# Kernel tuning notes

Measured on AMD Instinct MI355X. Metric: run time of the kernel, lower is better.

## Reference

```python
import jax, jax.numpy as jnp
import numpy as np

N_USERS = 50000
N_ENTITIES = 100000
N_EDGES = 2000000
NNZ = 1000000
N_REL = 17  # n_relations; weight has n_relations-1 = 16 rows
DIM = 64
N_HOPS = 3


def setup_inputs() -> dict:
    key = jax.random.key(0)
    ks = jax.random.split(key, 8)
    user_emb = jax.random.normal(ks[0], (N_USERS, DIM), dtype=jnp.float32)
    entity_emb = jax.random.normal(ks[1], (N_ENTITIES, DIM), dtype=jnp.float32)
    weight = jax.random.normal(ks[2], (N_REL - 1, DIM), dtype=jnp.float32)
    unmask = jax.random.uniform(ks[3], (N_EDGES,), dtype=jnp.float32)
    edge_index = jax.random.randint(ks[4], (2, N_EDGES), 0, N_ENTITIES, dtype=jnp.int64) if jax.config.jax_enable_x64 else jax.random.randint(ks[4], (2, N_EDGES), 0, N_ENTITIES).astype(jnp.int32)
    edge_type = jax.random.randint(ks[5], (N_EDGES,), 1, N_REL).astype(edge_index.dtype)
    interact_rows = jax.random.randint(ks[6], (NNZ,), 0, N_USERS).astype(edge_index.dtype)
    interact_cols = jax.random.randint(ks[7], (NNZ,), 0, N_ENTITIES).astype(edge_index.dtype)
    return {
        "user_emb": user_emb,
        "entity_emb": entity_emb,
        "weight": weight,
        "unmask": unmask,
        "edge_index": edge_index,
        "edge_type": edge_type,
        "interact_rows": interact_rows,
        "interact_cols": interact_cols,
    }


def _l2_normalize(x, eps=1e-12):
    # matches torch.nn.functional.normalize(dim=1)
    norm = jnp.sqrt(jnp.sum(x * x, axis=1, keepdims=True))
    return x / jnp.maximum(norm, eps)


def reference(user_emb, entity_emb, weight, unmask, edge_index, edge_type, interact_rows, interact_cols):
    """GraphConv.forward with mess_dropout=False, node_dropout=False (eval math)."""
    head = edge_index[0]
    tail = edge_index[1]
    rel_emb = weight[edge_type - 1]                      # [E, D] gather
    entity_res = entity_emb
    user_res = user_emb
    ent = entity_emb
    for _ in range(N_HOPS):
        # KG aggregate: gather-multiply-scatter_sum
        neigh = ent[tail] * unmask[:, None] * rel_emb    # [E, D]
        ent_agg = jax.ops.segment_sum(neigh, head, num_segments=N_ENTITIES)
        # user aggregate: sparse (unit-valued COO) mm -> gather + segment_sum
        usr_agg = jax.ops.segment_sum(ent[interact_cols], interact_rows, num_segments=N_USERS)
        ent = _l2_normalize(ent_agg)
        usr = _l2_normalize(usr_agg)
        entity_res = entity_res + ent
        user_res = user_res + usr
    return entity_res, user_res
```

## Files before the change

### kernel.cpp

```cpp
#include <hip/hip_runtime.h>
#include <hip/hip_fp16.h>
#include <math.h>

#define N_USERS   50000
#define N_ENT     100000
#define N_EDGES   2000000
#define NNZ       1000000
#define DIM       64
#define HALF_E    (N_ENT / 2)
#define HALF_U    (N_USERS / 2)

#define GA      512
#define NB_E    391
#define NB_U    196
#define NALL_E  (NB_E * GA)
#define NALL_U  (NB_U * GA)
#define NALL    (NALL_E + NALL_U)
#define NB_SCAN (NALL / 512)
#define CAP_D   6400


__device__ inline unsigned pack_h2(float x, float y) {
    unsigned lo = __half_as_ushort(__float2half_rn(x));
    unsigned hi = __half_as_ushort(__float2half_rn(y));
    return lo | (hi << 16);
}

__device__ inline float2 unpack_h2(unsigned u) {
    __half2 h = *reinterpret_cast<__half2*>(&u);
    return __half22float2(h);
}

__device__ inline __half2 bits_h2(unsigned u) { return *reinterpret_cast<__half2*>(&u); }

__device__ inline __half2 shfl_h2(__half2 v, int o) {
    int x = *reinterpret_cast<int*>(&v);
    x = __shfl_xor(x, o, 64);
    return *reinterpret_cast<__half2*>(&x);
}

__global__ void f32_to_f16(const float4* __restrict__ in, uint4* __restrict__ out, int n4) {
    int i = blockIdx.x * blockDim.x + threadIdx.x;
    if (i < n4) {
        float4 a = in[2 * i], b = in[2 * i + 1];
        uint4 o;
        o.x = pack_h2(a.x, a.y);
        o.y = pack_h2(a.z, a.w);
        o.z = pack_h2(b.x, b.y);
        o.w = pack_h2(b.z, b.w);
        out[i] = o;
    }
}


__global__ __launch_bounds__(256) void bucket_hist_both(
    const int* __restrict__ head, const int* __restrict__ irows, int* __restrict__ bh) {
    __shared__ int h[NB_E];
    bool isE = blockIdx.x < GA;
    int b = isE ? blockIdx.x : blockIdx.x - GA;
    const int* key = isE ? head : irows;
    int n = isE ? N_EDGES : NNZ;
    int nbuck = isE ? NB_E : NB_U;
    int base = isE ? 0 : NALL_E;
    for (int t = threadIdx.x; t < nbuck; t += 256) h[t] = 0;
    __syncthreads();
    int chunk = (n + GA - 1) / GA;
    int s = b * chunk;
    int e = n < s + chunk ? n : s + chunk;
    for (int i = s + threadIdx.x; i < e; i += 256)
        atomicAdd(&h[key[i] >> 8], 1);
    __syncthreads();
    for (int t = threadIdx.x; t < nbuck; t += 256)
        bh[base + t * GA + b] = h[t];
}

__global__ void scan_partial(const int* __restrict__ cnt, int n, int* __restrict__ bsum) {
    __shared__ int sd[512];
    int tid = threadIdx.x, i = blockIdx.x * 512 + tid;
    sd[tid] = (i < n) ? cnt[i] : 0;
    __syncthreads();
    for (int s = 256; s > 0; s >>= 1) {
        if (tid < s) sd[tid] += sd[tid + s];
        __syncthreads();
    }
    if (tid == 0) bsum[blockIdx.x] = sd[0];
}

__global__ void scan_bsum(int* bsum, int nb) {
    __shared__ int sd[1024];
    int tid = threadIdx.x;
    int v = (tid < nb) ? bsum[tid] : 0;
    sd[tid] = v;
    __syncthreads();
    for (int o = 1; o < 1024; o <<= 1) {
        int t = (tid >= o) ? sd[tid - o] : 0;
        __syncthreads();
        sd[tid] += t;
        __syncthreads();
    }
    if (tid < nb) bsum[tid] = sd[tid] - v;
}

__global__ void scan_final(const int* __restrict__ cnt, int n,
                           const int* __restrict__ bsum, int* __restrict__ rp) {
    __shared__ int sd[512];
    int tid = threadIdx.x, i = blockIdx.x * 512 + tid;
    int v = (i < n) ? cnt[i] : 0;
    sd[tid] = v;
    __syncthreads();
    for (int o = 1; o < 512; o <<= 1) {
        int t = (tid >= o) ? sd[tid - o] : 0;
        __syncthreads();
        sd[tid] += t;
        __syncthreads();
    }
    int incl = sd[tid] + bsum[blockIdx.x];
    if (i < n) rp[i] = incl - v;
    if (i == n - 1) rp[n] = incl;
}

__global__ __launch_bounds__(256) void bucket_scatter_both(
    const int* __restrict__ head, const int* __restrict__ tail,
    const int* __restrict__ etype, const float* __restrict__ unmask,
    const int* __restrict__ irows, const int* __restrict__ icols,
    const int* __restrict__ off, long long* __restrict__ tmp_ev,
    int* __restrict__ tmp_col) {
    __shared__ int h[NB_E];
    __shared__ int boff[NB_E];
    bool isE = blockIdx.x < GA;
    int b = isE ? blockIdx.x : blockIdx.x - GA;
    if (isE) {
        for (int t = threadIdx.x; t < NB_E; t += 256) { h[t] = 0; boff[t] = off[t * GA + b]; }
        __syncthreads();
        int chunk = (N_EDGES + GA - 1) / GA;
        int s = b * chunk;
        int e = N_EDGES < s + chunk ? N_EDGES : s + chunk;
        for (int i = s + threadIdx.x; i < e; i += 256) {
            int k = head[i];
            int bk = k >> 8;
            int local = atomicAdd(&h[bk], 1);
            unsigned hh = __half_as_ushort(__float2half_rn(unmask[i]));
            unsigned hi = hh | (hh << 16);
            unsigned lo = (unsigned)(tail[i] | ((etype[i] - 1) << 20) | ((k & 255) << 24));
            tmp_ev[boff[bk] + local] = (long long)(((unsigned long long)hi << 32) | lo);
        }
    } else {
        for (int t = threadIdx.x; t < NB_U; t += 256) { h[t] = 0; boff[t] = off[NALL_E + t * GA + b] - N_EDGES; }
        __syncthreads();
        int chunk = (NNZ + GA - 1) / GA;
        int s = b * chunk;
        int e = NNZ < s + chunk ? NNZ : s + chunk;
        for (int i = s + threadIdx.x; i < e; i += 256) {
            int k = irows[i];
            int bk = k >> 8;
            int local = atomicAdd(&h[bk], 1);
            tmp_col[boff[bk] + local] = icols[i] | ((k & 255) << 24);
        }
    }
}

__global__ __launch_bounds__(256) void bucket_sort_both(
    const int* __restrict__ off, const long long* __restrict__ tmp_ev,
    const int* __restrict__ tmp_col, long long* __restrict__ ev,
    int* __restrict__ col_s, int* __restrict__ rp_e, int* __restrict__ rp_u) {
    __shared__ int khist[256];
    __shared__ int koff[256];
    __shared__ long long stage[CAP_D];
    int t = threadIdx.x;
    bool isE = blockIdx.x < NB_E;
    if (isE) {
        int b = blockIdx.x;
        int sb = off[b * GA], se = off[(b + 1) * GA];
        int len = se - sb;
        khist[t] = 0;
        __syncthreads();
        for (int i = t; i < len; i += 256)
            atomicAdd(&khist[(int)(((unsigned long long)tmp_ev[sb + i] >> 24) & 255)], 1);
        __syncthreads();
        int v = khist[t];
        koff[t] = v;
        __syncthreads();
        for (int o = 1; o < 256; o <<= 1) {
            int x = (t >= o) ? koff[t - o] : 0;
            __syncthreads();
            koff[t] += x;
            __syncthreads();
        }
        int excl = koff[t] - v;
        int key = b * 256 + t;
        if (key < N_ENT) rp_e[key] = sb + excl;
        if (b == 0 && t == 0) rp_e[N_ENT] = N_EDGES;
        khist[t] = excl;
        __syncthreads();
        if (len <= CAP_D) {
            for (int i = t; i < len; i += 256) {
                long long v2 = tmp_ev[sb + i];
                int k = (int)(((unsigned long long)v2 >> 24) & 255);
                int p = atomicAdd(&khist[k], 1);
                stage[p] = v2;
            }
            __syncthreads();
            for (int i = t; i < len; i += 256)
                ev[sb + i] = stage[i] & (long long)0xFFFFFFFF00FFFFFFULL;
        } else {
            for (int i = t; i < len; i += 256) {
                long long v2 = tmp_ev[sb + i];
                int k = (int)(((unsigned long long)v2 >> 24) & 255);
                int p = atomicAdd(&khist[k], 1);
                ev[sb + p] = v2 & (long long)0xFFFFFFFF00FFFFFFULL;
            }
        }
    } else {
        int b = blockIdx.x - NB_E;
        int sb = off[NALL_E + b * GA] - N_EDGES;
        int se = off[NALL_E + (b + 1) * GA] - N_EDGES;
        int len = se - sb;
        int* stage32 = (int*)stage;
        khist[t] = 0;
        __syncthreads();
        for (int i = t; i < len; i += 256)
            atomicAdd(&khist[(tmp_col[sb + i] >> 24) & 255], 1);
        __syncthreads();
        int v = khist[t];
        koff[t] = v;
        __syncthreads();
        for (int o = 1; o < 256; o <<= 1) {
            int x = (t >= o) ? koff[t - o] : 0;
            __syncthreads();
            koff[t] += x;
            __syncthreads();
        }
        int excl = koff[t] - v;
        int key = b * 256 + t;
        if (key < N_USERS) rp_u[key] = sb + excl;
        if (b == 0 && t == 0) rp_u[N_USERS] = NNZ;
        khist[t] = excl;
        __syncthreads();
        if (len <= CAP_D) {
            for (int i = t; i < len; i += 256) {
                int v2 = tmp_col[sb + i];
                int p = atomicAdd(&khist[(v2 >> 24) & 255], 1);
                stage32[p] = v2;
            }
            __syncthreads();
            for (int i = t; i < len; i += 256)
                col_s[sb + i] = stage32[i] & 0x00FFFFFF;
        } else {
            for (int i = t; i < len; i += 256) {
                int v2 = tmp_col[sb + i];
                int p = atomicAdd(&khist[(v2 >> 24) & 255], 1);
                col_s[sb + p] = v2 & 0x00FFFFFF;
            }
        }
    }
}


__device__ inline void edge_body16(const uint4* __restrict__ in16,
                                   const uint4* __restrict__ w16,
                                   int ex, unsigned scbits, int sub, __half2 (&acc)[4]) {
    int tt = ex & 0xFFFFF, rt = (ex >> 20) & 15;
    uint4 r4 = in16[(size_t)tt * 8 + sub];
    uint4 w4 = w16[rt * 8 + sub];
    __half2 sc2 = bits_h2(scbits);
    acc[0] = __hfma2(__hmul2(bits_h2(r4.x), sc2), bits_h2(w4.x), acc[0]);
    acc[1] = __hfma2(__hmul2(bits_h2(r4.y), sc2), bits_h2(w4.y), acc[1]);
    acc[2] = __hfma2(__hmul2(bits_h2(r4.z), sc2), bits_h2(w4.z), acc[2]);
    acc[3] = __hfma2(__hmul2(bits_h2(r4.w), sc2), bits_h2(w4.w), acc[3]);
}

template <int FINAL>
__global__ __launch_bounds__(256) void agg_hop(
    const uint4* __restrict__ in16, const uint4* __restrict__ w16,
    const int* __restrict__ rp_e, const int2* __restrict__ ev,
    const int* __restrict__ rp_u, const int* __restrict__ col_s,
    uint4* __restrict__ oute, uint4* __restrict__ outu,
    const uint4* __restrict__ pe1, const uint4* __restrict__ pu1,
    const uint4* __restrict__ pu2,
    const float4* __restrict__ emb_e, const float4* __restrict__ emb_u,
    float4* __restrict__ res_e, float4* __restrict__ res_u) {
    int gwave = (blockIdx.x * blockDim.x + threadIdx.x) >> 6;
    if (gwave >= HALF_E + HALF_U) return;
    int lane = threadIdx.x & 63;
    int half = lane >> 5;
    int grp = (lane >> 3) & 3;
    int sub = lane & 7;

    bool is_ent = gwave < HALF_E;
    int row = is_ent ? gwave * 2 + half : (gwave - HALF_E) * 2 + half;
    const int* __restrict__ rp = is_ent ? rp_e : rp_u;
    int beg = rp[row], end = rp[row + 1];

    __half2 acc[4];
#pragma unroll
    for (int j = 0; j < 4; ++j) acc[j] = bits_h2(0u);

    if (is_ent) {
        for (int p0 = beg; p0 < end; p0 += 8) {
            int pA = p0 + grp, pB = p0 + 4 + grp;
            int2 eA = (pA < end) ? ev[pA] : make_int2(0, 0);
            int2 eB = (pB < end) ? ev[pB] : make_int2(0, 0);
            edge_body16(in16, w16, eA.x, (unsigned)eA.y, sub, acc);
            edge_body16(in16, w16, eB.x, (unsigned)eB.y, sub, acc);
        }
    } else {
        for (int p0 = beg; p0 < end; p0 += 8) {
            int pA = p0 + grp, pB = p0 + 4 + grp;
            int cA = 0, cB = 0;
            unsigned mAb = 0u, mBb = 0u;
            if (pA < end) { cA = col_s[pA]; mAb = 0x3C003C00u; }
            if (pB < end) { cB = col_s[pB]; mBb = 0x3C003C00u; }
            __half2 mA = bits_h2(mAb), mB = bits_h2(mBb);
            {
                uint4 r4 = in16[(size_t)cA * 8 + sub];
                acc[0] = __hfma2(bits_h2(r4.x), mA, acc[0]);
                acc[1] = __hfma2(bits_h2(r4.y), mA, acc[1]);
                acc[2] = __hfma2(bits_h2(r4.z), mA, acc[2]);
                acc[3] = __hfma2(bits_h2(r4.w), mA, acc[3]);
            }
            {
                uint4 r4 = in16[(size_t)cB * 8 + sub];
                acc[0] = __hfma2(bits_h2(r4.x), mB, acc[0]);
                acc[1] = __hfma2(bits_h2(r4.y), mB, acc[1]);
                acc[2] = __hfma2(bits_h2(r4.z), mB, acc[2]);
                acc[3] = __hfma2(bits_h2(r4.w), mB, acc[3]);
            }
        }
    }

#pragma unroll
    for (int j = 0; j < 4; ++j) {
        acc[j] = __hadd2(acc[j], shfl_h2(acc[j], 8));
        acc[j] = __hadd2(acc[j], shfl_h2(acc[j], 16));
    }
    float2 f0 = __half22float2(acc[0]), f1 = __half22float2(acc[1]);
    float2 f2 = __half22float2(acc[2]), f3 = __half22float2(acc[3]);
    float ss = f0.x * f0.x + f0.y * f0.y + f1.x * f1.x + f1.y * f1.y +
               f2.x * f2.x + f2.y * f2.y + f3.x * f3.x + f3.y * f3.y;
    ss += __shfl_xor(ss, 1, 64);
    ss += __shfl_xor(ss, 2, 64);
    ss += __shfl_xor(ss, 4, 64);
    float inv = 1.0f / fmaxf(sqrtf(ss), 1e-12f);

    if (grp == 0) {
        float n0 = f0.x * inv, n1 = f0.y * inv, n2 = f1.x * inv, n3 = f1.y * inv;
        float n4 = f2.x * inv, n5 = f2.y * inv, n6 = f3.x * inv, n7 = f3.y * inv;
        if constexpr (!FINAL) {
            uint4 p;
            p.x = pack_h2(n0, n1); p.y = pack_h2(n2, n3);
            p.z = pack_h2(n4, n5); p.w = pack_h2(n6, n7);
            (is_ent ? oute : outu)[(size_t)row * 8 + sub] = p;
        } else {
            const uint4* q1p = is_ent ? pe1 : pu1;
            const uint4* q2p = is_ent ? in16 : pu2;
            uint4 q1 = q1p[(size_t)row * 8 + sub];
            uint4 q2 = q2p[(size_t)row * 8 + sub];
            const float4* emb = is_ent ? emb_e : emb_u;
            float4* res = is_ent ? res_e : res_u;
            size_t rb = (size_t)row * 16 + sub * 2;
            float4 a = emb[rb], b = emb[rb + 1];
            float2 x0 = unpack_h2(q1.x), x1 = unpack_h2(q1.y);
            float2 x2 = unpack_h2(q1.z), x3 = unpack_h2(q1.w);
            float2 y0 = unpack_h2(q2.x), y1 = unpack_h2(q2.y);
            float2 y2 = unpack_h2(q2.z), y3 = unpack_h2(q2.w);
            a.x += n0 + x0.x + y0.x;  a.y += n1 + x0.y + y0.y;
            a.z += n2 + x1.x + y1.x;  a.w += n3 + x1.y + y1.y;
            b.x += n4 + x2.x + y2.x;  b.y += n5 + x2.y + y2.y;
            b.z += n6 + x3.x + y3.x;  b.w += n7 + x3.y + y3.y;
            res[rb] = a;
            res[rb + 1] = b;
        }
    }
}


extern "C" void kernel_launch(void* const* d_in, const int* in_sizes, int n_in,
                              void* d_out, int out_size, void* d_ws, size_t ws_size,
                              hipStream_t stream) {
    const float* user_emb   = (const float*)d_in[0];
    const float* entity_emb = (const float*)d_in[1];
    const float* weight     = (const float*)d_in[2];
    const float* unmask     = (const float*)d_in[3];
    const int*   edge_index = (const int*)d_in[4];
    const int*   edge_type  = (const int*)d_in[5];
    const int*   irows      = (const int*)d_in[6];
    const int*   icols      = (const int*)d_in[7];
    const int* head = edge_index;
    const int* tail = edge_index + N_EDGES;

    char* ws = (char*)d_ws;
    size_t off = 0;
    auto alloc = [&](size_t bytes) -> void* {
        void* p = ws + off;
        off += (bytes + 255) & ~(size_t)255;
        return p;
    };
    uint4* B0     = (uint4*)alloc((size_t)N_ENT * DIM * 2);
    uint4* B1     = (uint4*)alloc((size_t)N_ENT * DIM * 2);
    uint4* B2     = (uint4*)alloc((size_t)N_ENT * DIM * 2);
    uint4* U1     = (uint4*)alloc((size_t)N_USERS * DIM * 2);
    uint4* U2     = (uint4*)alloc((size_t)N_USERS * DIM * 2);
    uint4* w16    = (uint4*)alloc(16 * DIM * 2);
    int*   rp_e   = (int*)alloc((N_ENT + 1) * 4);
    int*   rp_u   = (int*)alloc((N_USERS + 1) * 4);
    long long* ev     = (long long*)alloc((size_t)N_EDGES * 8);
    long long* tmp_ev = (long long*)alloc((size_t)N_EDGES * 8);
    int*   col_s   = (int*)alloc((size_t)NNZ * 4);
    int*   tmp_col = (int*)alloc((size_t)NNZ * 4);
    int*   bh     = (int*)alloc((size_t)(NALL + 1) * 4);
    int*   offA   = (int*)alloc((size_t)(NALL + 1) * 4);
    int*   bs     = (int*)alloc(1024 * 4);
    (void)ws_size;

    f32_to_f16<<<(N_ENT * DIM / 8 + 255) / 256, 256, 0, stream>>>(
        (const float4*)entity_emb, B0, N_ENT * DIM / 8);
    f32_to_f16<<<1, 128, 0, stream>>>((const float4*)weight, w16, 16 * DIM / 8);

    bucket_hist_both<<<2 * GA, 256, 0, stream>>>(head, irows, bh);
    scan_partial<<<NB_SCAN, 512, 0, stream>>>(bh, NALL, bs);
    scan_bsum<<<1, 1024, 0, stream>>>(bs, NB_SCAN);
    scan_final<<<NB_SCAN, 512, 0, stream>>>(bh, NALL, bs, offA);
    bucket_scatter_both<<<2 * GA, 256, 0, stream>>>(
        head, tail, edge_type, unmask, irows, icols, offA, tmp_ev, tmp_col);
    bucket_sort_both<<<NB_E + NB_U, 256, 0, stream>>>(
        offA, tmp_ev, tmp_col, ev, col_s, rp_e, rp_u);

    float* res_e = (float*)d_out;
    float* res_u = res_e + (size_t)N_ENT * DIM;
    int grid_agg = ((HALF_E + HALF_U) * 64 + 255) / 256;

    agg_hop<0><<<grid_agg, 256, 0, stream>>>(
        B0, w16, rp_e, (const int2*)ev, rp_u, col_s, B1, U1,
        nullptr, nullptr, nullptr, nullptr, nullptr, nullptr, nullptr);
    agg_hop<0><<<grid_agg, 256, 0, stream>>>(
        B1, w16, rp_e, (const int2*)ev, rp_u, col_s, B2, U2,
        nullptr, nullptr, nullptr, nullptr, nullptr, nullptr, nullptr);
    agg_hop<1><<<grid_agg, 256, 0, stream>>>(
        B2, w16, rp_e, (const int2*)ev, rp_u, col_s, nullptr, nullptr,
        B1, U1, U2,
        (const float4*)entity_emb, (const float4*)user_emb,
        (float4*)res_e, (float4*)res_u);
}
```

Measured before the change: 248.1 us.

## Use grid-stride persistent waves and prefetch next edge indices in aggregation

The aggregation kernel becomes grid-stride over row-pair waves with a fixed grid of 2048 blocks instead of one wave per row pair. The inner loops software-prefetch the next iteration's edge/column indices before the gather-FMA work, so the index load latency overlaps the embedding gathers. The risk is that the fixed grid causes load imbalance across rows of varying degree, and the extra registers for the prefetched values may lower occupancy.

```diff
diff --git a/kernel.cpp b/kernel.cpp
--- a/kernel.cpp
+++ b/kernel.cpp
@@ -279,13 +279,14 @@
     const uint4* __restrict__ pu2,
     const float4* __restrict__ emb_e, const float4* __restrict__ emb_u,
     float4* __restrict__ res_e, float4* __restrict__ res_u) {
-    int gwave = (blockIdx.x * blockDim.x + threadIdx.x) >> 6;
-    if (gwave >= HALF_E + HALF_U) return;
     int lane = threadIdx.x & 63;
     int half = lane >> 5;
     int grp = (lane >> 3) & 3;
     int sub = lane & 7;
-
+    int wave0 = (blockIdx.x * blockDim.x + threadIdx.x) >> 6;
+    int wstep = (gridDim.x * blockDim.x) >> 6;
+
+    for (int gwave = wave0; gwave < HALF_E + HALF_U; gwave += wstep) {
     bool is_ent = gwave < HALF_E;
     int row = is_ent ? gwave * 2 + half : (gwave - HALF_E) * 2 + half;
     const int* __restrict__ rp = is_ent ? rp_e : rp_u;
@@ -296,20 +297,38 @@
     for (int j = 0; j < 4; ++j) acc[j] = bits_h2(0u);
 
     if (is_ent) {
+        int pA = beg + grp, pB = beg + 4 + grp;
+        int2 eA = (pA < end) ? ev[pA] : make_int2(0, 0);
+        int2 eB = (pB < end) ? ev[pB] : make_int2(0, 0);
         for (int p0 = beg; p0 < end; p0 += 8) {
-            int pA = p0 + grp, pB = p0 + 4 + grp;
-            int2 eA = (pA < end) ? ev[pA] : make_int2(0, 0);
-            int2 eB = (pB < end) ? ev[pB] : make_int2(0, 0);
+            int np0 = p0 + 8;
+            int2 nA = make_int2(0, 0), nB = make_int2(0, 0);
+            if (np0 < end) {
+                int q = np0 + grp;
+                nA = (q < end) ? ev[q] : make_int2(0, 0);
+                q = np0 + 4 + grp;
+                nB = (q < end) ? ev[q] : make_int2(0, 0);
+            }
             edge_body16(in16, w16, eA.x, (unsigned)eA.y, sub, acc);
             edge_body16(in16, w16, eB.x, (unsigned)eB.y, sub, acc);
+            eA = nA; eB = nB;
         }
     } else {
+        int pA = beg + grp, pB = beg + 4 + grp;
+        int cA = 0, cB = 0;
+        unsigned mAb = 0u, mBb = 0u;
+        if (pA < end) { cA = col_s[pA]; mAb = 0x3C003C00u; }
+        if (pB < end) { cB = col_s[pB]; mBb = 0x3C003C00u; }
         for (int p0 = beg; p0 < end; p0 += 8) {
-            int pA = p0 + grp, pB = p0 + 4 + grp;
-            int cA = 0, cB = 0;
-            unsigned mAb = 0u, mBb = 0u;
-            if (pA < end) { cA = col_s[pA]; mAb = 0x3C003C00u; }
-            if (pB < end) { cB = col_s[pB]; mBb = 0x3C003C00u; }
+            int np0 = p0 + 8;
+            int nA = 0, nB = 0;
+            unsigned nmA = 0u, nmB = 0u;
+            if (np0 < end) {
+                int q = np0 + grp;
+                if (q < end) { nA = col_s[q]; nmA = 0x3C003C00u; }
+                q = np0 + 4 + grp;
+                if (q < end) { nB = col_s[q]; nmB = 0x3C003C00u; }
+            }
             __half2 mA = bits_h2(mAb), mB = bits_h2(mBb);
             {
                 uint4 r4 = in16[(size_t)cA * 8 + sub];
@@ -325,6 +344,7 @@
                 acc[2] = __hfma2(bits_h2(r4.z), mB, acc[2]);
                 acc[3] = __hfma2(bits_h2(r4.w), mB, acc[3]);
             }
+            cA = nA; cB = nB; mAb = nmA; mBb = nmB;
         }
     }
 
@@ -371,6 +391,7 @@
             res[rb + 1] = b;
         }
     }
+    }
 }
 
 
@@ -427,7 +448,7 @@
 
     float* res_e = (float*)d_out;
     float* res_u = res_e + (size_t)N_ENT * DIM;
-    int grid_agg = ((HALF_E + HALF_U) * 64 + 255) / 256;
+    int grid_agg = 2048;
 
     agg_hop<0><<<grid_agg, 256, 0, stream>>>(
         B0, w16, rp_e, (const int2*)ev, rp_u, col_s, B1, U1,
```

Result: no change. 251.0 us (+1.2%).
